# Kernel tuning notes

Hardware: AMD Instinct MI355X
Metric: run time of the kernel (lower is better)

Reference implementation:

```python
import jax, jax.numpy as jnp
import numpy as np
import math

D_MODEL, D_K, D_V, H = 512, 64, 64, 8

def setup_inputs() -> dict:
    key = jax.random.key(0)
    ks = jax.random.split(key, 8)
    B, L = 2, 4096
    q = jax.random.normal(ks[0], (B, L, D_MODEL), dtype=jnp.float32)
    k = jax.random.normal(ks[1], (B, L, D_MODEL), dtype=jnp.float32)
    v = jax.random.normal(ks[2], (B, L, D_MODEL), dtype=jnp.float32)
    attention_mask = jnp.ones((B, L), dtype=jnp.int32)
    s = 1.0 / math.sqrt(D_MODEL)
    Wq = jax.random.uniform(ks[3], (D_MODEL, H * D_K), dtype=jnp.float32, minval=-s, maxval=s)
    Wk = jax.random.uniform(ks[4], (D_MODEL, H * D_K), dtype=jnp.float32, minval=-s, maxval=s)
    Wv = jax.random.uniform(ks[5], (D_MODEL, H * D_V), dtype=jnp.float32, minval=-s, maxval=s)
    so = 1.0 / math.sqrt(H * D_V)
    Wo = jax.random.uniform(ks[6], (H * D_V, D_MODEL), dtype=jnp.float32, minval=-so, maxval=so)
    return {"q": q, "k": k, "v": v, "attention_mask": attention_mask,
            "Wq": Wq, "Wk": Wk, "Wv": Wv, "Wo": Wo}

def reference(q, k, v, attention_mask, Wq, Wk, Wv, Wo):
    B, L, _ = q.shape
    scale = 1.0 / math.sqrt(D_K)
    # project and split heads: [B, H, L, d]
    qh = (q @ Wq).reshape(B, L, H, D_K).transpose(0, 2, 1, 3)
    kh = (k @ Wk).reshape(B, L, H, D_K).transpose(0, 2, 1, 3)
    vh = (v @ Wv).reshape(B, L, H, D_V).transpose(0, 2, 1, 3)
    score = jnp.einsum('bhqd,bhkd->bhqk', qh, kh) * scale  # [B,H,L,L]
    mask = attention_mask[:, None, None, :]  # [B,1,1,L]
    score = jnp.where(mask == 0, -jnp.inf, score)
    attn = jax.nn.softmax(score, axis=-1)
    out = jnp.einsum('bhqk,bhkd->bhqd', attn, vh)
    out = out.transpose(0, 2, 1, 3).reshape(B, L, H * D_V)
    return out @ Wo
```

## Files before the change

### kernel.cpp

```cpp
#include <hip/hip_runtime.h>

typedef short bf16x8 __attribute__((ext_vector_type(8)));
typedef float f32x4 __attribute__((ext_vector_type(4)));
typedef unsigned short u16x8 __attribute__((ext_vector_type(8)));

static __device__ __forceinline__ unsigned short f2bf(float f) {
  unsigned int x = __builtin_bit_cast(unsigned int, f);
  x += 0x7FFFu + ((x >> 16) & 1u);
  return (unsigned short)(x >> 16);
}
static __device__ __forceinline__ unsigned int pk2bf(float a, float b) {
  unsigned int ia = __builtin_bit_cast(unsigned int, a) + 0x8000u;
  unsigned int ib = __builtin_bit_cast(unsigned int, b) + 0x8000u;
  return __builtin_amdgcn_perm(ib, ia, 0x07060302u);
}
static __device__ __forceinline__ unsigned int cvtpk(float a, float b) {
  unsigned int r;
  asm("v_cvt_pk_bf16_f32 %0, %1, %2" : "=v"(r) : "v"(a), "v"(b));
  return r;
}
static __device__ __forceinline__ void gl2lds16(const unsigned short* g, unsigned short* l) {
  __builtin_amdgcn_global_load_lds(
      (const __attribute__((address_space(1))) unsigned int*)g,
      (__attribute__((address_space(3))) unsigned int*)l, 16, 0, 0);
}

__global__ __launch_bounds__(256) void cvt3(const float* __restrict__ q, const float* __restrict__ k,
                                            const float* __restrict__ v,
                                            unsigned short* __restrict__ qo, unsigned short* __restrict__ ko,
                                            unsigned short* __restrict__ vo) {
  const float* src = (blockIdx.y == 0) ? q : (blockIdx.y == 1) ? k : v;
  unsigned short* dst = (blockIdx.y == 0) ? qo : (blockIdx.y == 1) ? ko : vo;
  int i = (blockIdx.x * 256 + threadIdx.x) * 8;
  float4 a = *(const float4*)(src + i);
  float4 b = *(const float4*)(src + i + 4);
  uint4 pk;
  pk.x = pk2bf(a.x, a.y); pk.y = pk2bf(a.z, a.w);
  pk.z = pk2bf(b.x, b.y); pk.w = pk2bf(b.z, b.w);
  *(uint4*)(dst + i) = pk;
}

__global__ __launch_bounds__(256) void wtrans4(const float* __restrict__ Wq, const float* __restrict__ Wk,
                                               const float* __restrict__ Wv, const float* __restrict__ Wo,
                                               unsigned short* __restrict__ WT) {
  __shared__ __align__(16) float T[64 * 68];
  const int z = blockIdx.z;
  const float* W = (z == 0) ? Wq : (z == 1) ? Wk : (z == 2) ? Wv : Wo;
  unsigned short* out = WT + (size_t)z * 512 * 512;
  const int k0 = blockIdx.x * 64, n0 = blockIdx.y * 64;
  const int tid = threadIdx.x;
#pragma unroll
  for (int i = 0; i < 4; ++i) {
    int chunk = i * 256 + tid;
    int row = chunk >> 4, fc = chunk & 15;
    *(float4*)(T + row * 68 + fc * 4) =
        *(const float4*)(W + (size_t)(k0 + row) * 512 + n0 + fc * 4);
  }
  __syncthreads();
#pragma unroll
  for (int i = 0; i < 2; ++i) {
    int chunk = i * 256 + tid;
    int nr = chunk >> 3, kc = chunk & 7;
    u16x8 v;
#pragma unroll
    for (int j = 0; j < 8; ++j) v[j] = f2bf(T[(kc * 8 + j) * 68 + nr]);
    *(u16x8*)(out + (size_t)(n0 + nr) * 512 + k0 + kc * 8) = v;
  }
}

__global__ __launch_bounds__(256) void gemm_qkv(const unsigned short* __restrict__ Aq,
                                                const unsigned short* __restrict__ Ak,
                                                const unsigned short* __restrict__ Av,
                                                const unsigned short* __restrict__ Bt,
                                                unsigned short* __restrict__ C,
                                                float qscale) {
  __shared__ __align__(16) unsigned short Abuf[2][128 * 32];
  __shared__ __align__(16) unsigned short Bbuf[2][128 * 32];
  const int K = 512, LDC = 1536;
  const unsigned short* A = (blockIdx.y < 4) ? Aq : (blockIdx.y < 8) ? Ak : Av;
  const float scale = (blockIdx.y < 4) ? qscale : 1.0f;
  const int tid = threadIdx.x;
  const int wid = tid >> 6, lane = tid & 63, quad = lane >> 4, li = lane & 15;
  const int bm = blockIdx.x * 128, bn = blockIdx.y * 128;
  const int wr = (wid >> 1) * 64, wc = (wid & 1) * 64;

  const unsigned short* ga[2]; int oa[2];
  const unsigned short* gb[2]; int ob[2];
#pragma unroll
  for (int i = 0; i < 2; ++i) {
    int lam = i * 256 + tid;
    int r = lam >> 2, c = (lam & 3) ^ (r & 3);
    ga[i] = A + (size_t)(bm + r) * K + c * 8;
    gb[i] = Bt + (size_t)(bn + r) * K + c * 8;
    oa[i] = lam * 8;
    ob[i] = lam * 8;
  }
#pragma unroll
  for (int i = 0; i < 2; ++i) { gl2lds16(ga[i], &Abuf[0][oa[i]]); ga[i] += 32; }
#pragma unroll
  for (int i = 0; i < 2; ++i) { gl2lds16(gb[i], &Bbuf[0][ob[i]]); gb[i] += 32; }

  f32x4 acc[4][4] = {};
  const int xo = (quad ^ (li & 3)) * 8;
  for (int s = 0; s < 16; ++s) {
    __builtin_amdgcn_s_barrier();
    if (s + 1 < 16) {
      int p = (s + 1) & 1;
#pragma unroll
      for (int i = 0; i < 2; ++i) { gl2lds16(ga[i], &Abuf[p][oa[i]]); ga[i] += 32; }
#pragma unroll
      for (int i = 0; i < 2; ++i) { gl2lds16(gb[i], &Bbuf[p][ob[i]]); gb[i] += 32; }
      asm volatile("s_waitcnt vmcnt(4)" ::: "memory");
    } else {
      asm volatile("s_waitcnt vmcnt(0)" ::: "memory");
    }
    __builtin_amdgcn_s_barrier();
    __builtin_amdgcn_sched_barrier(0);
    const unsigned short* As = &Abuf[s & 1][0];
    const unsigned short* Bs = &Bbuf[s & 1][0];
    bf16x8 af[4], bf[4];
#pragma unroll
    for (int t = 0; t < 4; ++t)
      af[t] = *(const bf16x8*)(As + (wr + t * 16 + li) * 32 + xo);
#pragma unroll
    for (int t = 0; t < 4; ++t)
      bf[t] = *(const bf16x8*)(Bs + (wc + t * 16 + li) * 32 + xo);
#pragma unroll
    for (int mt = 0; mt < 4; ++mt)
#pragma unroll
      for (int nt = 0; nt < 4; ++nt)
        acc[mt][nt] = __builtin_amdgcn_mfma_f32_16x16x32_bf16(af[mt], bf[nt], acc[mt][nt], 0, 0, 0);
  }
#pragma unroll
  for (int mt = 0; mt < 4; ++mt)
#pragma unroll
    for (int nt = 0; nt < 4; ++nt) {
      int r0 = bm + wr + mt * 16 + quad * 4;
      int c  = bn + wc + nt * 16 + li;
#pragma unroll
      for (int r = 0; r < 4; ++r)
        C[(size_t)(r0 + r) * LDC + c] = f2bf(acc[mt][nt][r] * scale);
    }
}

__global__ __launch_bounds__(256) void gemm_o(const unsigned short* __restrict__ A,
                                              const unsigned short* __restrict__ Bt,
                                              float* __restrict__ Cf) {
  __shared__ __align__(16) unsigned short Abuf[2][128 * 64];
  __shared__ __align__(16) unsigned short Bbuf[2][64 * 64];
  const int K = 512, LDC = 512;
  const int tid = threadIdx.x;
  const int wid = tid >> 6, lane = tid & 63, quad = lane >> 4, li = lane & 15;
  const int bm = blockIdx.x * 128, bn = blockIdx.y * 64;
  const int wm = wid * 32;
  const unsigned short* ga[4]; int oa[4];
  const unsigned short* gb[2]; int ob[2];
#pragma unroll
  for (int i = 0; i < 4; ++i) {
    int lam = i * 256 + wid * 64 + lane;
    int r = lam >> 3, c = (lam & 7) ^ (r & 7);
    ga[i] = A + (size_t)(bm + r) * K + c * 8;
    oa[i] = lam * 8;
  }
#pragma unroll
  for (int i = 0; i < 2; ++i) {
    int lam = i * 256 + wid * 64 + lane;
    int r = lam >> 3, c = (lam & 7) ^ (r & 7);
    gb[i] = Bt + (size_t)(bn + r) * K + c * 8;
    ob[i] = lam * 8;
  }
#pragma unroll
  for (int i = 0; i < 4; ++i) { gl2lds16(ga[i], &Abuf[0][oa[i]]); ga[i] += 64; }
#pragma unroll
  for (int i = 0; i < 2; ++i) { gl2lds16(gb[i], &Bbuf[0][ob[i]]); gb[i] += 64; }

  f32x4 acc[2][4] = {};
  const int sw = li & 7;
  for (int s = 0; s < 8; ++s) {
    __builtin_amdgcn_s_barrier();
    if (s + 1 < 8) {
      int p = (s + 1) & 1;
#pragma unroll
      for (int i = 0; i < 4; ++i) { gl2lds16(ga[i], &Abuf[p][oa[i]]); ga[i] += 64; }
#pragma unroll
      for (int i = 0; i < 2; ++i) { gl2lds16(gb[i], &Bbuf[p][ob[i]]); gb[i] += 64; }
      asm volatile("s_waitcnt vmcnt(6)" ::: "memory");
    } else {
      asm volatile("s_waitcnt vmcnt(0)" ::: "memory");
    }
    __builtin_amdgcn_s_barrier();
    __builtin_amdgcn_sched_barrier(0);
    const unsigned short* As = &Abuf[s & 1][0];
    const unsigned short* Bs = &Bbuf[s & 1][0];
#pragma unroll
    for (int kk = 0; kk < 2; ++kk) {
      bf16x8 af[2], bfr[4];
#pragma unroll
      for (int t = 0; t < 2; ++t)
        af[t] = *(const bf16x8*)(As + (wm + t * 16 + li) * 64 + (((kk * 4 + quad) ^ sw) * 8));
#pragma unroll
      for (int t = 0; t < 4; ++t)
        bfr[t] = *(const bf16x8*)(Bs + (t * 16 + li) * 64 + (((kk * 4 + quad) ^ sw) * 8));
#pragma unroll
      for (int mt = 0; mt < 2; ++mt)
#pragma unroll
        for (int nt = 0; nt < 4; ++nt)
          acc[mt][nt] = __builtin_amdgcn_mfma_f32_16x16x32_bf16(af[mt], bfr[nt], acc[mt][nt], 0, 0, 0);
    }
  }
#pragma unroll
  for (int mt = 0; mt < 2; ++mt)
#pragma unroll
    for (int nt = 0; nt < 4; ++nt) {
      int r0 = bm + wm + mt * 16 + quad * 4;
      int c  = bn + nt * 16 + li;
#pragma unroll
      for (int r = 0; r < 4; ++r)
        Cf[(size_t)(r0 + r) * LDC + c] = acc[mt][nt][r];
    }
}

__global__ __launch_bounds__(256) void vtrans(const unsigned short* __restrict__ qkv,
                                              unsigned short* __restrict__ vt) {
  __shared__ __align__(16) unsigned short T[64 * 72];
  const int kt = blockIdx.x;
  const int bh = blockIdx.y;
  const int b = bh >> 3, h = bh & 7;
  const int tid = threadIdx.x;
#pragma unroll
  for (int i = 0; i < 2; ++i) {
    int chunk = i * 256 + tid;
    int row = chunk >> 3, c8 = chunk & 7;
    *(uint4*)(T + row * 72 + c8 * 8) =
        *(const uint4*)(qkv + (size_t)(b * 4096 + kt * 64 + row) * 1536 + 1024 + h * 64 + c8 * 8);
  }
  __syncthreads();
#pragma unroll
  for (int i = 0; i < 2; ++i) {
    int chunk = i * 256 + tid;
    int dr = chunk >> 3, c8 = chunk & 7;
    u16x8 v;
#pragma unroll
    for (int j = 0; j < 8; ++j) {
      int p = c8 * 8 + j;
      int ph = p & 31;
      int lk = (p & 32) | (((ph >> 2) & 1) << 4) | (((ph >> 3) & 3) << 2) | (ph & 3);
      v[j] = T[lk * 72 + dr];
    }
    *(u16x8*)(vt + (size_t)(bh * 64 + dr) * 4096 + kt * 64 + c8 * 8) = v;
  }
}

__global__ __launch_bounds__(512, 2) void attn(const unsigned short* __restrict__ qkv,
                                               const unsigned short* __restrict__ vt,
                                               const int* __restrict__ mask,
                                               unsigned short* __restrict__ obuf) {
  __shared__ __align__(16) unsigned short SM[33024];
  unsigned short* Kb = SM;
  unsigned short* Vb = SM + 16384;
  unsigned short* Mk = SM + 32768;
  const int qt = blockIdx.x, h = blockIdx.y, b = blockIdx.z;
  const int tid = threadIdx.x;
  const int wid = tid >> 6, lane = tid & 63, quad = lane >> 4, li = lane & 15;
  const int hv = wid >> 2;
  const int wq = wid & 3;
  const size_t tok0 = (size_t)b * 4096;

  if (tid < 256) {
    const int4* mp = (const int4*)(mask + b * 4096 + tid * 16);
    unsigned int bits = 0;
#pragma unroll
    for (int j = 0; j < 4; ++j) {
      int4 m4 = mp[j];
      bits |= (m4.x ? 1u : 0u) << (j * 4 + 0);
      bits |= (m4.y ? 1u : 0u) << (j * 4 + 1);
      bits |= (m4.z ? 1u : 0u) << (j * 4 + 2);
      bits |= (m4.w ? 1u : 0u) << (j * 4 + 3);
    }
    Mk[tid] = (unsigned short)bits;
  }

  const unsigned short* qp0 = qkv + (tok0 + qt * 128 + wq * 32 + li) * 1536 + h * 64;
  const unsigned short* qp1 = qp0 + (size_t)16 * 1536;
  bf16x8 bq[2][2];
  bq[0][0] = *(const bf16x8*)(qp0 + quad * 8);
  bq[0][1] = *(const bf16x8*)(qp0 + 32 + quad * 8);
  bq[1][0] = *(const bf16x8*)(qp1 + quad * 8);
  bq[1][1] = *(const bf16x8*)(qp1 + 32 + quad * 8);

  const unsigned short* kbase = qkv + tok0 * 1536 + 512 + h * 64;
  const unsigned short* vbase = vt + (size_t)(b * 8 + h) * 64 * 4096;
  const int sr = tid >> 3, sc8 = ((tid & 7) ^ (sr & 7)) * 8;
  const unsigned short* gk0 = kbase + (size_t)sr * 1536 + sc8;
  const unsigned short* gk1 = kbase + (size_t)(2048 + sr) * 1536 + sc8;
  const unsigned short* gv0 = vbase + (size_t)sr * 4096 + sc8;
  const unsigned short* gv1 = vbase + (size_t)sr * 4096 + 2048 + sc8;
  const int ol = tid * 8;

  gl2lds16(gk0, Kb + ol);          gl2lds16(gk1, Kb + 4096 + ol);
  gl2lds16(gv0, Vb + ol);          gl2lds16(gv1, Vb + 4096 + ol);
  gk0 += (size_t)64 * 1536; gk1 += (size_t)64 * 1536; gv0 += 64; gv1 += 64;

  f32x4 lacc[2] = {};
  f32x4 accO[2][4] = {};
  const int sw = li & 7;

  asm volatile("s_waitcnt lgkmcnt(0)" ::: "memory");

  for (int t = 0; t < 32; ++t) {
    __builtin_amdgcn_s_barrier();
    if (t < 31) {
      int p = (t + 1) & 1;
      unsigned short* kd = Kb + p * 8192;
      unsigned short* vd = Vb + p * 8192;
      gl2lds16(gk0, kd + ol);        gl2lds16(gk1, kd + 4096 + ol);
      gl2lds16(gv0, vd + ol);        gl2lds16(gv1, vd + 4096 + ol);
      gk0 += (size_t)64 * 1536; gk1 += (size_t)64 * 1536; gv0 += 64; gv1 += 64;
      asm volatile("s_waitcnt vmcnt(4)" ::: "memory");
    } else {
      asm volatile("s_waitcnt vmcnt(0)" ::: "memory");
    }
    __builtin_amdgcn_s_barrier();
    __builtin_amdgcn_sched_barrier(0);
    const unsigned short* Ks = Kb + (t & 1) * 8192 + hv * 4096;
    const unsigned short* Vs = Vb + (t & 1) * 8192 + hv * 4096;

    f32x4 s[2][4];
    __builtin_amdgcn_s_setprio(1);
#pragma unroll
    for (int kb = 0; kb < 4; ++kb) {
      const unsigned short* kr = Ks + (kb * 16 + li) * 64;
      bf16x8 ak0 = *(const bf16x8*)(kr + ((quad ^ sw) * 8));
      bf16x8 ak1 = *(const bf16x8*)(kr + (((4 + quad) ^ sw) * 8));
#pragma unroll
      for (int qg = 0; qg < 2; ++qg) {
        f32x4 z = {};
        z = __builtin_amdgcn_mfma_f32_16x16x32_bf16(ak0, bq[qg][0], z, 0, 0, 0);
        z = __builtin_amdgcn_mfma_f32_16x16x32_bf16(ak1, bq[qg][1], z, 0, 0, 0);
        s[qg][kb] = z;
      }
    }
    __builtin_amdgcn_s_setprio(0);
    int tt = hv * 32 + t;
    unsigned long long mbits = *(const unsigned long long*)(Mk + tt * 4);
    if (mbits != ~0ull) {
#pragma unroll
      for (int kb = 0; kb < 4; ++kb)
#pragma unroll
        for (int r = 0; r < 4; ++r) {
          int key = kb * 16 + quad * 4 + r;
          if (!((mbits >> key) & 1ull)) { s[0][kb][r] = -1e30f; s[1][kb][r] = -1e30f; }
        }
    }
    bf16x8 pf[2][2];
#pragma unroll
    for (int qg = 0; qg < 2; ++qg) {
#pragma unroll
      for (int kb = 0; kb < 4; ++kb) {
#pragma unroll
        for (int r = 0; r < 4; ++r) s[qg][kb][r] = __builtin_amdgcn_exp2f(s[qg][kb][r]);
        lacc[qg] += s[qg][kb];
      }
      uint4 u0, u1;
      u0.x = cvtpk(s[qg][0][0], s[qg][0][1]); u0.y = cvtpk(s[qg][0][2], s[qg][0][3]);
      u0.z = cvtpk(s[qg][1][0], s[qg][1][1]); u0.w = cvtpk(s[qg][1][2], s[qg][1][3]);
      u1.x = cvtpk(s[qg][2][0], s[qg][2][1]); u1.y = cvtpk(s[qg][2][2], s[qg][2][3]);
      u1.z = cvtpk(s[qg][3][0], s[qg][3][1]); u1.w = cvtpk(s[qg][3][2], s[qg][3][3]);
      pf[qg][0] = __builtin_bit_cast(bf16x8, u0);
      pf[qg][1] = __builtin_bit_cast(bf16x8, u1);
    }
    __builtin_amdgcn_s_setprio(1);
#pragma unroll
    for (int dc = 0; dc < 4; ++dc) {
      const unsigned short* vr = Vs + (dc * 16 + li) * 64;
      bf16x8 bv0 = *(const bf16x8*)(vr + ((quad ^ sw) * 8));
      bf16x8 bv1 = *(const bf16x8*)(vr + (((4 + quad) ^ sw) * 8));
#pragma unroll
      for (int qg = 0; qg < 2; ++qg) {
        accO[qg][dc] = __builtin_amdgcn_mfma_f32_16x16x32_bf16(pf[qg][0], bv0, accO[qg][dc], 0, 0, 0);
        accO[qg][dc] = __builtin_amdgcn_mfma_f32_16x16x32_bf16(pf[qg][1], bv1, accO[qg][dc], 0, 0, 0);
      }
    }
    __builtin_amdgcn_s_setprio(0);
  }

  __syncthreads();
  float* scr = (float*)SM;
  if (hv == 1) {
#pragma unroll
    for (int qg = 0; qg < 2; ++qg) {
#pragma unroll
      for (int dc = 0; dc < 4; ++dc)
#pragma unroll
        for (int r = 0; r < 4; ++r)
          scr[(qg * 16 + dc * 4 + r) * 256 + wq * 64 + lane] = accO[qg][dc][r];
#pragma unroll
      for (int r = 0; r < 4; ++r)
        scr[(32 + qg * 4 + r) * 256 + wq * 64 + lane] = lacc[qg][r];
    }
  }
  __syncthreads();
  if (hv == 0) {
#pragma unroll
    for (int qg = 0; qg < 2; ++qg) {
#pragma unroll
      for (int dc = 0; dc < 4; ++dc)
#pragma unroll
        for (int r = 0; r < 4; ++r)
          accO[qg][dc][r] += scr[(qg * 16 + dc * 4 + r) * 256 + wq * 64 + lane];
#pragma unroll
      for (int r = 0; r < 4; ++r)
        lacc[qg][r] += scr[(32 + qg * 4 + r) * 256 + wq * 64 + lane];
    }
#pragma unroll
    for (int qg = 0; qg < 2; ++qg) {
      float lt = lacc[qg][0] + lacc[qg][1] + lacc[qg][2] + lacc[qg][3];
      lt += __shfl_xor(lt, 16);
      lt += __shfl_xor(lt, 32);
      float lv0 = 1.f / __shfl(lt, quad * 4 + 0);
      float lv1 = 1.f / __shfl(lt, quad * 4 + 1);
      float lv2 = 1.f / __shfl(lt, quad * 4 + 2);
      float lv3 = 1.f / __shfl(lt, quad * 4 + 3);
      size_t r0q = tok0 + qt * 128 + wq * 32 + qg * 16 + quad * 4;
#pragma unroll
      for (int dc = 0; dc < 4; ++dc) {
        size_t col = h * 64 + dc * 16 + li;
        obuf[(r0q + 0) * 512 + col] = f2bf(accO[qg][dc][0] * lv0);
        obuf[(r0q + 1) * 512 + col] = f2bf(accO[qg][dc][1] * lv1);
        obuf[(r0q + 2) * 512 + col] = f2bf(accO[qg][dc][2] * lv2);
        obuf[(r0q + 3) * 512 + col] = f2bf(accO[qg][dc][3] * lv3);
      }
    }
  }
}

extern "C" void kernel_launch(void* const* d_in, const int* in_sizes, int n_in,
                              void* d_out, int out_size, void* d_ws, size_t ws_size,
                              hipStream_t stream) {
  const float* q  = (const float*)d_in[0];
  const float* k  = (const float*)d_in[1];
  const float* v  = (const float*)d_in[2];
  const int* mask = (const int*)d_in[3];
  const float* Wq = (const float*)d_in[4];
  const float* Wk = (const float*)d_in[5];
  const float* Wv = (const float*)d_in[6];
  const float* Wo = (const float*)d_in[7];
  float* out = (float*)d_out;

  char* ws = (char*)d_ws;
  const size_t SA = (size_t)8192 * 512 * 2;
  unsigned short* qbf  = (unsigned short*)(ws);
  unsigned short* kbf  = (unsigned short*)(ws + SA);
  unsigned short* vbf  = (unsigned short*)(ws + 2 * SA);
  unsigned short* qkvh = (unsigned short*)(ws + 3 * SA);
  unsigned short* wAll = (unsigned short*)(ws + 6 * SA);
  unsigned short* woT  = wAll + (size_t)3 * 512 * 512;
  unsigned short* vtb  = qbf;
  unsigned short* ob   = kbf;

  dim3 cg(2048, 3);
  cvt3<<<cg, 256, 0, stream>>>(q, k, v, qbf, kbf, vbf);
  dim3 wg(8, 8, 4);
  wtrans4<<<wg, 256, 0, stream>>>(Wq, Wk, Wv, Wo, wAll);
  const float qscale = 0.125f * 1.44269504f;
  dim3 gq(64, 12);
  gemm_qkv<<<gq, 256, 0, stream>>>(qbf, kbf, vbf, wAll, qkvh, qscale);
  dim3 vg(64, 16);
  vtrans<<<vg, 256, 0, stream>>>(qkvh, vtb);
  dim3 ag(32, 8, 2);
  attn<<<ag, 512, 0, stream>>>(qkvh, vtb, mask, ob);
  dim3 go(64, 8);
  gemm_o<<<go, 256, 0, stream>>>(ob, woT, out);
}
```

Measured before the change: 216.9 us.

## Fuse fp32-to-bf16 conversion and V transpose into QKV projection GEMM

Removes the separate cvt3 conversion kernel by having gemm_qkv load fp32 activations directly, pack them to bf16 in registers, and store them into LDS with a one-stage register prefetch. It also removes the vtrans kernel by having the V-projection blocks write their output straight into the transposed, permuted layout the attention kernel expects. Two launches and the intermediate bf16 buffer round trips go away. In exchange the A-tile loads now go through registers instead of direct global-to-LDS loads, which needs more careful waitcnt bookkeeping, and the transposed V store uses narrower 8-byte scattered writes.

```diff
diff --git a/kernel.cpp b/kernel.cpp
--- a/kernel.cpp
+++ b/kernel.cpp
@@ -23,21 +23,6 @@
   __builtin_amdgcn_global_load_lds(
       (const __attribute__((address_space(1))) unsigned int*)g,
       (__attribute__((address_space(3))) unsigned int*)l, 16, 0, 0);
-}
-
-__global__ __launch_bounds__(256) void cvt3(const float* __restrict__ q, const float* __restrict__ k,
-                                            const float* __restrict__ v,
-                                            unsigned short* __restrict__ qo, unsigned short* __restrict__ ko,
-                                            unsigned short* __restrict__ vo) {
-  const float* src = (blockIdx.y == 0) ? q : (blockIdx.y == 1) ? k : v;
-  unsigned short* dst = (blockIdx.y == 0) ? qo : (blockIdx.y == 1) ? ko : vo;
-  int i = (blockIdx.x * 256 + threadIdx.x) * 8;
-  float4 a = *(const float4*)(src + i);
-  float4 b = *(const float4*)(src + i + 4);
-  uint4 pk;
-  pk.x = pk2bf(a.x, a.y); pk.y = pk2bf(a.z, a.w);
-  pk.z = pk2bf(b.x, b.y); pk.w = pk2bf(b.z, b.w);
-  *(uint4*)(dst + i) = pk;
 }
 
 __global__ __launch_bounds__(256) void wtrans4(const float* __restrict__ Wq, const float* __restrict__ Wk,
@@ -68,37 +53,51 @@
   }
 }
 
-__global__ __launch_bounds__(256) void gemm_qkv(const unsigned short* __restrict__ Aq,
-                                                const unsigned short* __restrict__ Ak,
-                                                const unsigned short* __restrict__ Av,
+__global__ __launch_bounds__(256) void gemm_qkv(const float* __restrict__ Aq,
+                                                const float* __restrict__ Ak,
+                                                const float* __restrict__ Av,
                                                 const unsigned short* __restrict__ Bt,
                                                 unsigned short* __restrict__ C,
+                                                unsigned short* __restrict__ vt,
                                                 float qscale) {
   __shared__ __align__(16) unsigned short Abuf[2][128 * 32];
   __shared__ __align__(16) unsigned short Bbuf[2][128 * 32];
   const int K = 512, LDC = 1536;
-  const unsigned short* A = (blockIdx.y < 4) ? Aq : (blockIdx.y < 8) ? Ak : Av;
-  const float scale = (blockIdx.y < 4) ? qscale : 1.0f;
+  const int y = blockIdx.y;
+  const float* A32 = (y < 4) ? Aq : (y < 8) ? Ak : Av;
   const int tid = threadIdx.x;
   const int wid = tid >> 6, lane = tid & 63, quad = lane >> 4, li = lane & 15;
-  const int bm = blockIdx.x * 128, bn = blockIdx.y * 128;
+  const int bm = blockIdx.x * 128, bn = y * 128;
   const int wr = (wid >> 1) * 64, wc = (wid & 1) * 64;
 
-  const unsigned short* ga[2]; int oa[2];
-  const unsigned short* gb[2]; int ob[2];
-#pragma unroll
-  for (int i = 0; i < 2; ++i) {
-    int lam = i * 256 + tid;
-    int r = lam >> 2, c = (lam & 3) ^ (r & 3);
-    ga[i] = A + (size_t)(bm + r) * K + c * 8;
-    gb[i] = Bt + (size_t)(bn + r) * K + c * 8;
-    oa[i] = lam * 8;
-    ob[i] = lam * 8;
-  }
-#pragma unroll
-  for (int i = 0; i < 2; ++i) { gl2lds16(ga[i], &Abuf[0][oa[i]]); ga[i] += 32; }
-#pragma unroll
-  for (int i = 0; i < 2; ++i) { gl2lds16(gb[i], &Bbuf[0][ob[i]]); gb[i] += 32; }
+  const int r0c = tid >> 2,         c0 = (tid & 3) ^ (r0c & 3);
+  const int r1c = (256 + tid) >> 2, c1 = ((256 + tid) & 3) ^ (r1c & 3);
+  const float* ga0 = A32 + (size_t)(bm + r0c) * K + c0 * 8;
+  const float* ga1 = A32 + (size_t)(bm + r1c) * K + c1 * 8;
+  const unsigned short* gb0 = Bt + (size_t)(bn + r0c) * K + c0 * 8;
+  const unsigned short* gb1 = Bt + (size_t)(bn + r1c) * K + c1 * 8;
+  const int oa0 = tid * 8, oa1 = (256 + tid) * 8;
+
+  float4 a0a = *(const float4*)(ga0);
+  float4 a0b = *(const float4*)(ga0 + 4);
+  float4 a1a = *(const float4*)(ga1);
+  float4 a1b = *(const float4*)(ga1 + 4);
+  ga0 += 32; ga1 += 32;
+  asm volatile("s_waitcnt vmcnt(0)" ::: "memory");
+  {
+    uint4 w0, w1;
+    w0.x = pk2bf(a0a.x, a0a.y); w0.y = pk2bf(a0a.z, a0a.w);
+    w0.z = pk2bf(a0b.x, a0b.y); w0.w = pk2bf(a0b.z, a0b.w);
+    w1.x = pk2bf(a1a.x, a1a.y); w1.y = pk2bf(a1a.z, a1a.w);
+    w1.z = pk2bf(a1b.x, a1b.y); w1.w = pk2bf(a1b.z, a1b.w);
+    *(uint4*)(&Abuf[0][oa0]) = w0;
+    *(uint4*)(&Abuf[0][oa1]) = w1;
+  }
+  a0a = *(const float4*)(ga0); a0b = *(const float4*)(ga0 + 4);
+  a1a = *(const float4*)(ga1); a1b = *(const float4*)(ga1 + 4);
+  ga0 += 32; ga1 += 32;
+  gl2lds16(gb0, &Bbuf[0][oa0]); gl2lds16(gb1, &Bbuf[0][oa1]);
+  gb0 += 32; gb1 += 32;
 
   f32x4 acc[4][4] = {};
   const int xo = (quad ^ (li & 3)) * 8;
@@ -106,14 +105,26 @@
     __builtin_amdgcn_s_barrier();
     if (s + 1 < 16) {
       int p = (s + 1) & 1;
-#pragma unroll
-      for (int i = 0; i < 2; ++i) { gl2lds16(ga[i], &Abuf[p][oa[i]]); ga[i] += 32; }
-#pragma unroll
-      for (int i = 0; i < 2; ++i) { gl2lds16(gb[i], &Bbuf[p][ob[i]]); gb[i] += 32; }
-      asm volatile("s_waitcnt vmcnt(4)" ::: "memory");
-    } else {
-      asm volatile("s_waitcnt vmcnt(0)" ::: "memory");
-    }
+      asm volatile("s_waitcnt vmcnt(2)" ::: "memory");
+      uint4 w0, w1;
+      w0.x = pk2bf(a0a.x, a0a.y); w0.y = pk2bf(a0a.z, a0a.w);
+      w0.z = pk2bf(a0b.x, a0b.y); w0.w = pk2bf(a0b.z, a0b.w);
+      w1.x = pk2bf(a1a.x, a1a.y); w1.y = pk2bf(a1a.z, a1a.w);
+      w1.z = pk2bf(a1b.x, a1b.y); w1.w = pk2bf(a1b.z, a1b.w);
+      *(uint4*)(&Abuf[p][oa0]) = w0;
+      *(uint4*)(&Abuf[p][oa1]) = w1;
+      if (s + 2 < 16) {
+        a0a = *(const float4*)(ga0); a0b = *(const float4*)(ga0 + 4);
+        a1a = *(const float4*)(ga1); a1b = *(const float4*)(ga1 + 4);
+        ga0 += 32; ga1 += 32;
+      }
+      gl2lds16(gb0, &Bbuf[p][oa0]); gl2lds16(gb1, &Bbuf[p][oa1]);
+      gb0 += 32; gb1 += 32;
+    }
+    if (s <= 13)      asm volatile("s_waitcnt vmcnt(6)" ::: "memory");
+    else if (s == 14) asm volatile("s_waitcnt vmcnt(2)" ::: "memory");
+    else              asm volatile("s_waitcnt vmcnt(0)" ::: "memory");
+    asm volatile("s_waitcnt lgkmcnt(0)" ::: "memory");
     __builtin_amdgcn_s_barrier();
     __builtin_amdgcn_sched_barrier(0);
     const unsigned short* As = &Abuf[s & 1][0];
@@ -131,16 +142,36 @@
       for (int nt = 0; nt < 4; ++nt)
         acc[mt][nt] = __builtin_amdgcn_mfma_f32_16x16x32_bf16(af[mt], bf[nt], acc[mt][nt], 0, 0, 0);
   }
-#pragma unroll
-  for (int mt = 0; mt < 4; ++mt)
-#pragma unroll
-    for (int nt = 0; nt < 4; ++nt) {
-      int r0 = bm + wr + mt * 16 + quad * 4;
-      int c  = bn + wc + nt * 16 + li;
-#pragma unroll
-      for (int r = 0; r < 4; ++r)
-        C[(size_t)(r0 + r) * LDC + c] = f2bf(acc[mt][nt][r] * scale);
-    }
+
+  if (y < 8) {
+    const float scale = (y < 4) ? qscale : 1.0f;
+#pragma unroll
+    for (int mt = 0; mt < 4; ++mt)
+#pragma unroll
+      for (int nt = 0; nt < 4; ++nt) {
+        int r0 = bm + wr + mt * 16 + quad * 4;
+        int c  = bn + wc + nt * 16 + li;
+#pragma unroll
+        for (int r = 0; r < 4; ++r)
+          C[(size_t)(r0 + r) * LDC + c] = f2bf(acc[mt][nt][r] * scale);
+      }
+  } else {
+    const int tile_g = (bm + wr) >> 6;
+    const int bb = tile_g >> 6, kt = tile_g & 63;
+#pragma unroll
+    for (int mt = 0; mt < 4; ++mt) {
+      int pb = (mt >> 1) * 32 + quad * 8 + (mt & 1) * 4;
+#pragma unroll
+      for (int nt = 0; nt < 4; ++nt) {
+        int col = bn + wc + nt * 16 + li - 1024;
+        int hh = col >> 6, dd = col & 63;
+        uint2 w;
+        w.x = (unsigned int)f2bf(acc[mt][nt][0]) | ((unsigned int)f2bf(acc[mt][nt][1]) << 16);
+        w.y = (unsigned int)f2bf(acc[mt][nt][2]) | ((unsigned int)f2bf(acc[mt][nt][3]) << 16);
+        *(uint2*)(vt + ((size_t)(bb * 8 + hh) * 64 + dd) * 4096 + kt * 64 + pb) = w;
+      }
+    }
+  }
 }
 
 __global__ __launch_bounds__(256) void gemm_o(const unsigned short* __restrict__ A,
@@ -218,37 +249,6 @@
       for (int r = 0; r < 4; ++r)
         Cf[(size_t)(r0 + r) * LDC + c] = acc[mt][nt][r];
     }
-}
-
-__global__ __launch_bounds__(256) void vtrans(const unsigned short* __restrict__ qkv,
-                                              unsigned short* __restrict__ vt) {
-  __shared__ __align__(16) unsigned short T[64 * 72];
-  const int kt = blockIdx.x;
-  const int bh = blockIdx.y;
-  const int b = bh >> 3, h = bh & 7;
-  const int tid = threadIdx.x;
-#pragma unroll
-  for (int i = 0; i < 2; ++i) {
-    int chunk = i * 256 + tid;
-    int row = chunk >> 3, c8 = chunk & 7;
-    *(uint4*)(T + row * 72 + c8 * 8) =
-        *(const uint4*)(qkv + (size_t)(b * 4096 + kt * 64 + row) * 1536 + 1024 + h * 64 + c8 * 8);
-  }
-  __syncthreads();
-#pragma unroll
-  for (int i = 0; i < 2; ++i) {
-    int chunk = i * 256 + tid;
-    int dr = chunk >> 3, c8 = chunk & 7;
-    u16x8 v;
-#pragma unroll
-    for (int j = 0; j < 8; ++j) {
-      int p = c8 * 8 + j;
-      int ph = p & 31;
-      int lk = (p & 32) | (((ph >> 2) & 1) << 4) | (((ph >> 3) & 3) << 2) | (ph & 3);
-      v[j] = T[lk * 72 + dr];
-    }
-    *(u16x8*)(vt + (size_t)(bh * 64 + dr) * 4096 + kt * 64 + c8 * 8) = v;
-  }
 }
 
 __global__ __launch_bounds__(512, 2) void attn(const unsigned short* __restrict__ qkv,
@@ -449,24 +449,17 @@
 
   char* ws = (char*)d_ws;
   const size_t SA = (size_t)8192 * 512 * 2;
-  unsigned short* qbf  = (unsigned short*)(ws);
-  unsigned short* kbf  = (unsigned short*)(ws + SA);
-  unsigned short* vbf  = (unsigned short*)(ws + 2 * SA);
+  unsigned short* vtb  = (unsigned short*)(ws);
+  unsigned short* ob   = (unsigned short*)(ws + SA);
   unsigned short* qkvh = (unsigned short*)(ws + 3 * SA);
   unsigned short* wAll = (unsigned short*)(ws + 6 * SA);
   unsigned short* woT  = wAll + (size_t)3 * 512 * 512;
-  unsigned short* vtb  = qbf;
-  unsigned short* ob   = kbf;
-
-  dim3 cg(2048, 3);
-  cvt3<<<cg, 256, 0, stream>>>(q, k, v, qbf, kbf, vbf);
+
   dim3 wg(8, 8, 4);
   wtrans4<<<wg, 256, 0, stream>>>(Wq, Wk, Wv, Wo, wAll);
   const float qscale = 0.125f * 1.44269504f;
   dim3 gq(64, 12);
-  gemm_qkv<<<gq, 256, 0, stream>>>(qbf, kbf, vbf, wAll, qkvh, qscale);
-  dim3 vg(64, 16);
-  vtrans<<<vg, 256, 0, stream>>>(qkvh, vtb);
+  gemm_qkv<<<gq, 256, 0, stream>>>(q, k, v, wAll, qkvh, vtb, qscale);
   dim3 ag(32, 8, 2);
   attn<<<ag, 512, 0, stream>>>(qkvh, vtb, mask, ob);
   dim3 go(64, 8);
```

New measurement: 219.1 us. Within noise of the previous version (+1.0%).
